# Performance work log

Measured on AMD Instinct MI355X. Metric: run time of the kernel, lower is better.

The kernel has to match this reference:

```python
import jax, jax.numpy as jnp
import numpy as np

N_NODES = 100000
N_EDGES = 3200000
IN_C = 128
OUT_C = 40
NEG_SLOPE = 0.2


def _p(key, shape, scale=0.1):
    return jax.random.normal(key, shape, dtype=jnp.float32) * scale


def setup_inputs() -> dict:
    key = jax.random.key(0)
    ks = jax.random.split(key, 16)
    x = jax.random.normal(ks[0], (N_NODES, IN_C), dtype=jnp.float32)
    edge_index = jax.random.randint(ks[1], (2, N_EDGES), 0, N_NODES, dtype=jnp.int32)
    # layer 1: in=128 -> heads=4, out=4 (concat -> 16)
    W1 = _p(ks[2], (IN_C, 4 * 4))
    a_src1 = _p(ks[3], (4, 4))
    a_dst1 = _p(ks[4], (4, 4))
    b1 = jnp.zeros((16,), jnp.float32)
    # layer 2: 16 -> heads=8, out=8 (concat -> 64)
    W2 = _p(ks[5], (16, 8 * 8))
    a_src2 = _p(ks[6], (8, 8))
    a_dst2 = _p(ks[7], (8, 8))
    b2 = jnp.zeros((64,), jnp.float32)
    # layer 3: 64 -> heads=1, out=OUT_C, concat=False
    W3 = _p(ks[8], (64, OUT_C))
    a_src3 = _p(ks[9], (1, OUT_C))
    a_dst3 = _p(ks[10], (1, OUT_C))
    b3 = jnp.zeros((OUT_C,), jnp.float32)
    return {"x": x, "edge_index": edge_index,
            "W1": W1, "a_src1": a_src1, "a_dst1": a_dst1, "b1": b1,
            "W2": W2, "a_src2": a_src2, "a_dst2": a_dst2, "b2": b2,
            "W3": W3, "a_src3": a_src3, "a_dst3": a_dst3, "b3": b3}


def gat_conv(x, src, dst, W, a_src, a_dst, b, heads, out_c, concat):
    # x: [N, F_in]; src/dst: [E] (self loops already included)
    N = x.shape[0]
    h = (x @ W).reshape(N, heads, out_c)                 # [N, H, C]
    e_src = jnp.sum(h * a_src, axis=-1)                  # [N, H]
    e_dst = jnp.sum(h * a_dst, axis=-1)                  # [N, H]
    e = jax.nn.leaky_relu(e_src[src] + e_dst[dst], NEG_SLOPE)  # [E, H]
    # segment softmax over edges grouped by destination node
    m = jax.ops.segment_max(e, dst, num_segments=N)      # [N, H]
    ex = jnp.exp(e - m[dst])
    s = jax.ops.segment_sum(ex, dst, num_segments=N)
    alpha = ex / (s[dst] + 1e-16)                        # [E, H]
    out = jax.ops.segment_sum(h[src] * alpha[:, :, None], dst, num_segments=N)  # [N, H, C]
    out = out.reshape(N, heads * out_c) if concat else out.mean(axis=1)
    return out + b


def reference(x, edge_index, W1, a_src1, a_dst1, b1, W2, a_src2, a_dst2, b2, W3, a_src3, a_dst3, b3):
    N = x.shape[0]
    loops = jnp.arange(N, dtype=edge_index.dtype)
    src = jnp.concatenate([edge_index[0], loops])
    dst = jnp.concatenate([edge_index[1], loops])
    h = jax.nn.elu(gat_conv(x, src, dst, W1, a_src1, a_dst1, b1, 4, 4, True))
    h = jax.nn.elu(gat_conv(h, src, dst, W2, a_src2, a_dst2, b2, 8, 8, True))
    out = gat_conv(h, src, dst, W3, a_src3, a_dst3, b3, 1, OUT_C, False)
    return out
```

## Files before the change

kernel.cpp:

```cpp
#include <hip/hip_runtime.h>

#define NN 100000
#define NE 3200000
#define ET (NE + NN)
#define NEG_SLOPE 0.2f
#define BSH 7
#define WIN (1 << BSH)
#define NBUC ((NN + WIN - 1) >> BSH)
#define NBLK 256
#define EPB ((ET + NBLK - 1) / NBLK)

__device__ __host__ __forceinline__ int swz(int b) {
    return (b & 7) * (NBLK / 8) + (b >> 3);
}

__device__ __forceinline__ float lrelu(float v) { return v > 0.f ? v : NEG_SLOPE * v; }

__device__ __forceinline__ unsigned short f2bf(float x) {
    unsigned u = __float_as_uint(x);
    return (unsigned short)((u + 0x7fffu + ((u >> 16) & 1u)) >> 16);
}
__device__ __forceinline__ float bflo(unsigned u) { return __uint_as_float(u << 16); }
__device__ __forceinline__ float bfhi(unsigned u) { return __uint_as_float(u & 0xffff0000u); }


template <int FIN, int FOUT, int C>
__device__ __forceinline__ void gemm_attn_body(
    int idx, const float* __restrict__ x, const float* Ws,
    const float* __restrict__ a_src, const float* __restrict__ a_dst,
    unsigned short* __restrict__ h, float* __restrict__ esrc,
    float* __restrict__ edst, int N) {
    constexpr int HH = FOUT / C;
    constexpr int F4 = FOUT / 4;
    constexpr int TPH = C / 4;
    if (idx >= N * F4) return;
    int n = idx / F4, f4 = idx - n * F4;
    int fb = 4 * f4;
    const float4* xr = (const float4*)(x + (long)n * FIN);
    float a0 = 0.f, a1 = 0.f, a2 = 0.f, a3 = 0.f;
#pragma unroll
    for (int k4 = 0; k4 < FIN / 4; ++k4) {
        float4 xv = xr[k4];
        const float* wr = &Ws[(4 * k4) * FOUT + fb];
        float4 w0 = *(const float4*)(wr);
        float4 w1 = *(const float4*)(wr + FOUT);
        float4 w2 = *(const float4*)(wr + 2 * FOUT);
        float4 w3 = *(const float4*)(wr + 3 * FOUT);
        a0 = fmaf(xv.x, w0.x, a0); a1 = fmaf(xv.x, w0.y, a1);
        a2 = fmaf(xv.x, w0.z, a2); a3 = fmaf(xv.x, w0.w, a3);
        a0 = fmaf(xv.y, w1.x, a0); a1 = fmaf(xv.y, w1.y, a1);
        a2 = fmaf(xv.y, w1.z, a2); a3 = fmaf(xv.y, w1.w, a3);
        a0 = fmaf(xv.z, w2.x, a0); a1 = fmaf(xv.z, w2.y, a1);
        a2 = fmaf(xv.z, w2.z, a2); a3 = fmaf(xv.z, w2.w, a3);
        a0 = fmaf(xv.w, w3.x, a0); a1 = fmaf(xv.w, w3.y, a1);
        a2 = fmaf(xv.w, w3.z, a2); a3 = fmaf(xv.w, w3.w, a3);
    }
    unsigned short b0 = f2bf(a0), b1 = f2bf(a1), b2 = f2bf(a2), b3 = f2bf(a3);
    *(ushort4*)(h + (long)n * FOUT + fb) = make_ushort4(b0, b1, b2, b3);
    float q0 = bflo((unsigned)b0), q1 = bflo((unsigned)b1);
    float q2 = bflo((unsigned)b2), q3 = bflo((unsigned)b3);
    float vs = q0 * a_src[fb] + q1 * a_src[fb + 1] + q2 * a_src[fb + 2] + q3 * a_src[fb + 3];
    float vd = q0 * a_dst[fb] + q1 * a_dst[fb + 1] + q2 * a_dst[fb + 2] + q3 * a_dst[fb + 3];
#pragma unroll
    for (int o = 1; o < TPH; o <<= 1) {
        vs += __shfl_xor(vs, o);
        vd += __shfl_xor(vd, o);
    }
    if ((f4 % TPH) == 0) {
        int hh = f4 / TPH;
        esrc[n * HH + hh] = vs;
        edst[n * HH + hh] = vd;
    }
}


__global__ __launch_bounds__(256) void cntgemm_kernel(
    const int* __restrict__ dst, int* __restrict__ cnt,
    const float* __restrict__ x, const float* __restrict__ W,
    const float* __restrict__ a_src, const float* __restrict__ a_dst,
    unsigned short* __restrict__ h, float* __restrict__ esrc,
    float* __restrict__ edst, int N) {
    __shared__ __align__(16) char smem[128 * 16 * 4];
    if (blockIdx.x < NBLK) {
        int* hh = (int*)smem;
        for (int i = threadIdx.x; i < NBUC; i += 256) hh[i] = 0;
        __syncthreads();
        int lo = blockIdx.x * EPB;
        int hi = lo + EPB; if (hi > ET) hi = ET;
        for (int k = lo + threadIdx.x; k < hi; k += 256) {
            int d = (k < NE) ? dst[k] : k - NE;
            atomicAdd(&hh[d >> BSH], 1);
        }
        __syncthreads();
        int col = swz(blockIdx.x);
        for (int i = threadIdx.x; i < NBUC; i += 256)
            cnt[i * NBLK + col] = hh[i];
    } else {
        float* Ws = (float*)smem;
        for (int i = threadIdx.x; i < 128 * 16; i += 256) Ws[i] = W[i];
        __syncthreads();
        int idx = (blockIdx.x - NBLK) * 256 + threadIdx.x;
        gemm_attn_body<128, 16, 4>(idx, x, Ws, a_src, a_dst, h, esrc, edst, N);
    }
}


__global__ __launch_bounds__(256) void rowsum_kernel(const int* __restrict__ cnt,
                                                     int* __restrict__ tot) {
    int wave = threadIdx.x >> 6, lane = threadIdx.x & 63;
    int b = blockIdx.x * 4 + wave;
    if (b >= NBUC) return;
    int4 v = ((const int4*)(cnt + b * NBLK))[lane];
    int s = v.x + v.y + v.z + v.w;
#pragma unroll
    for (int off = 32; off; off >>= 1) s += __shfl_xor(s, off);
    if (lane == 0) tot[b] = s;
}

__global__ __launch_bounds__(1024) void scan_kernel(const int* __restrict__ tot,
                                                    int* __restrict__ bstart) {
    __shared__ int t[1024];
    int b = threadIdx.x;
    int s = (b < NBUC) ? tot[b] : 0;
    t[b] = s;
    __syncthreads();
    for (int off = 1; off < 1024; off <<= 1) {
        int v = (b >= off) ? t[b - off] : 0;
        __syncthreads();
        t[b] += v;
        __syncthreads();
    }
    if (b < NBUC) bstart[b] = t[b] - s;
    if (b == 0) bstart[NBUC] = ET;
}

__global__ __launch_bounds__(256) void base_kernel(int* __restrict__ cnt,
                                                   const int* __restrict__ bstart) {
    int wave = threadIdx.x >> 6, lane = threadIdx.x & 63;
    int b = blockIdx.x * 4 + wave;
    if (b >= NBUC) return;
    int run = bstart[b];
    for (int c0 = 0; c0 < NBLK; c0 += 64) {
        int v = cnt[b * NBLK + c0 + lane];
        int x = v;
#pragma unroll
        for (int off = 1; off < 64; off <<= 1) {
            int y = __shfl_up(x, off);
            if (lane >= off) x += y;
        }
        cnt[b * NBLK + c0 + lane] = run + x - v;
        run += __shfl(x, 63);
    }
}

__global__ __launch_bounds__(1024) void scatter_kernel(const int* __restrict__ src,
                                                       const int* __restrict__ dst,
                                                       const int* __restrict__ base,
                                                       unsigned* __restrict__ tmpp) {
    __shared__ int loff[NBUC];
    int col = swz(blockIdx.x);
    for (int i = threadIdx.x; i < NBUC; i += 1024) loff[i] = base[i * NBLK + col];
    __syncthreads();
    int lo = blockIdx.x * EPB;
    int hi = lo + EPB; if (hi > ET) hi = ET;
    for (int k = lo + threadIdx.x; k < hi; k += 1024) {
        int s, d;
        if (k < NE) { s = src[k]; d = dst[k]; }
        else { s = d = k - NE; }
        int p = atomicAdd(&loff[d >> BSH], 1);
        tmpp[p] = (unsigned)s | ((unsigned)(d & (WIN - 1)) << 17);
    }
}

__global__ __launch_bounds__(1024) void sort_kernel(const int* __restrict__ bstart,
                                                    const unsigned* __restrict__ tmpp,
                                                    int* __restrict__ rowptr,
                                                    int* __restrict__ ssrc) {
    __shared__ int hist[WIN];
    __shared__ int scan[WIN];
    __shared__ int cur[WIN];
    int buc = blockIdx.x;
    int nlo = buc << BSH;
    int nwin = NN - nlo; if (nwin > WIN) nwin = WIN;
    int lo = bstart[buc], hi = bstart[buc + 1];
    int tid = threadIdx.x;
    if (tid < WIN) hist[tid] = 0;
    __syncthreads();
    for (int k = lo + tid; k < hi; k += 1024)
        atomicAdd(&hist[tmpp[k] >> 17], 1);
    __syncthreads();
    if (tid < WIN) scan[tid] = hist[tid];
    __syncthreads();
    for (int off = 1; off < WIN; off <<= 1) {
        int v = (tid >= off && tid < WIN) ? scan[tid - off] : 0;
        __syncthreads();
        if (tid < WIN) scan[tid] += v;
        __syncthreads();
    }
    if (tid < WIN) {
        int ex = scan[tid] - hist[tid];
        cur[tid] = ex;
        if (tid < nwin) rowptr[nlo + tid] = lo + ex;
    }
    if (buc == 0 && tid == 0) rowptr[NN] = ET;
    __syncthreads();
    for (int k = lo + tid; k < hi; k += 1024) {
        unsigned e = tmpp[k];
        int p = atomicAdd(&cur[e >> 17], 1);
        ssrc[lo + p] = (int)(e & 0x1FFFFu);
    }
}


template <int FIN, int FOUT, int C>
__global__ __launch_bounds__(256) void gemm_attn_kernel(
    const float* __restrict__ x, const float* __restrict__ W,
    const float* __restrict__ a_src, const float* __restrict__ a_dst,
    unsigned short* __restrict__ h, float* __restrict__ esrc,
    float* __restrict__ edst, int N) {
    __shared__ __align__(16) float Ws[FIN * FOUT];
    for (int i = threadIdx.x; i < FIN * FOUT; i += blockDim.x) Ws[i] = W[i];
    __syncthreads();
    int idx = blockIdx.x * blockDim.x + threadIdx.x;
    gemm_attn_body<FIN, FOUT, C>(idx, x, Ws, a_src, a_dst, h, esrc, edst, N);
}

template <int FIN, int FOUT, int SO>
__global__ __launch_bounds__(256) void gemm_kernel(const float* __restrict__ x,
                                                   const float* __restrict__ W,
                                                   unsigned short* __restrict__ h, int N) {
    constexpr int F4 = FOUT / 4;
    __shared__ __align__(16) float Ws[FIN * FOUT];
    for (int i = threadIdx.x; i < FIN * FOUT; i += blockDim.x) Ws[i] = W[i];
    __syncthreads();
    int idx = blockIdx.x * blockDim.x + threadIdx.x;
    if (idx >= N * F4) return;
    int n = idx / F4, f4 = idx - n * F4;
    int fb = 4 * f4;
    const float4* xr = (const float4*)(x + (long)n * FIN);
    float a0 = 0.f, a1 = 0.f, a2 = 0.f, a3 = 0.f;
#pragma unroll
    for (int k4 = 0; k4 < FIN / 4; ++k4) {
        float4 xv = xr[k4];
        const float* wr = &Ws[(4 * k4) * FOUT + fb];
        float4 w0 = *(const float4*)(wr);
        float4 w1 = *(const float4*)(wr + FOUT);
        float4 w2 = *(const float4*)(wr + 2 * FOUT);
        float4 w3 = *(const float4*)(wr + 3 * FOUT);
        a0 = fmaf(xv.x, w0.x, a0); a1 = fmaf(xv.x, w0.y, a1);
        a2 = fmaf(xv.x, w0.z, a2); a3 = fmaf(xv.x, w0.w, a3);
        a0 = fmaf(xv.y, w1.x, a0); a1 = fmaf(xv.y, w1.y, a1);
        a2 = fmaf(xv.y, w1.z, a2); a3 = fmaf(xv.y, w1.w, a3);
        a0 = fmaf(xv.z, w2.x, a0); a1 = fmaf(xv.z, w2.y, a1);
        a2 = fmaf(xv.z, w2.z, a2); a3 = fmaf(xv.z, w2.w, a3);
        a0 = fmaf(xv.w, w3.x, a0); a1 = fmaf(xv.w, w3.y, a1);
        a2 = fmaf(xv.w, w3.z, a2); a3 = fmaf(xv.w, w3.w, a3);
    }
    *(ushort4*)(h + (long)n * SO + fb) = make_ushort4(f2bf(a0), f2bf(a1), f2bf(a2), f2bf(a3));
}

template <int C, int SO>
__global__ void attn_kernel(const unsigned short* __restrict__ h,
                            const float* __restrict__ a_src,
                            const float* __restrict__ a_dst, float* __restrict__ esrc,
                            float* __restrict__ edst, int N) {
    int idx = blockIdx.x * blockDim.x + threadIdx.x;
    if (idx >= N) return;
    const uint4* hp = (const uint4*)(h + (long)idx * SO);
    float s = 0.f, d = 0.f;
#pragma unroll
    for (int c8 = 0; c8 < C / 8; ++c8) {
        uint4 v = hp[c8];
        int c = 8 * c8;
        s += bflo(v.x) * a_src[c] + bfhi(v.x) * a_src[c + 1];
        d += bflo(v.x) * a_dst[c] + bfhi(v.x) * a_dst[c + 1];
        s += bflo(v.y) * a_src[c + 2] + bfhi(v.y) * a_src[c + 3];
        d += bflo(v.y) * a_dst[c + 2] + bfhi(v.y) * a_dst[c + 3];
        s += bflo(v.z) * a_src[c + 4] + bfhi(v.z) * a_src[c + 5];
        d += bflo(v.z) * a_dst[c + 4] + bfhi(v.z) * a_dst[c + 5];
        s += bflo(v.w) * a_src[c + 6] + bfhi(v.w) * a_src[c + 7];
        d += bflo(v.w) * a_dst[c + 6] + bfhi(v.w) * a_dst[c + 7];
    }
    esrc[idx] = s;
    edst[idx] = d;
}

template <int H, int C, int L, int G, int NPW, int FPL, int RSL, int U, bool ELU>
__global__ __launch_bounds__(256) void agg_kernel(
    const int* __restrict__ rowptr, const int* __restrict__ ssrc,
    const float* __restrict__ esrc, const float* __restrict__ edst,
    const unsigned short* __restrict__ hbuf, const float* __restrict__ b,
    float* __restrict__ out, int N) {
    constexpr int F = H * C;
    constexpr int AQ = (F + FPL - 1) / FPL;
    constexpr int S = L * G;
    static_assert(S * NPW == 64, "wave layout");
    static_assert(AQ <= L, "lanes cover features");
    int lane = threadIdx.x & 63;
    int wave = threadIdx.x >> 6;
    int sub = lane / S;
    int ls = lane - sub * S;
    int g = ls / L, q = ls - g * L;
    int n = (blockIdx.x * 4 + wave) * NPW + sub;
    if (n >= N) return;
    const bool act = (q < AQ);
    int h = act ? (FPL * q) / C : 0;
    int qa = act ? q : 0;
    float edn = edst[n * H + h];
    int beg = rowptr[n], end = rowptr[n + 1];
    int kend = end - 1;
    float sum = 0.f;
    float acc[FPL];
#pragma unroll
    for (int i = 0; i < FPL; ++i) acc[i] = 0.f;

    int k = beg + g;
    int ss[U];
#pragma unroll
    for (int u = 0; u < U; ++u) {
        int kk = k + u * G;
        ss[u] = ssrc[kk < kend ? kk : kend];
    }
    while (k < end) {
        uint4 hv4[U];
        uint2 hv2[U];
        float es[U];
#pragma unroll
        for (int u = 0; u < U; ++u) {
            if constexpr (FPL == 8) hv4[u] = ((const uint4*)hbuf)[ss[u] * RSL + qa];
            else hv2[u] = ((const uint2*)hbuf)[ss[u] * RSL + qa];
            es[u] = esrc[ss[u] * H + h];
        }
        int kn = k + U * G;
        int sn[U];
#pragma unroll
        for (int u = 0; u < U; ++u) {
            int kk = kn + u * G;
            sn[u] = ssrc[kk < kend ? kk : kend];
        }
        __builtin_amdgcn_sched_barrier(0);
#pragma unroll
        for (int u = 0; u < U; ++u) {
            float ex = (act && (k + u * G < end)) ? __expf(lrelu(es[u] + edn)) : 0.f;
            if constexpr (FPL == 8) {
                uint4 v = hv4[u];
                acc[0] = fmaf(ex, bflo(v.x), acc[0]); acc[1] = fmaf(ex, bfhi(v.x), acc[1]);
                acc[2] = fmaf(ex, bflo(v.y), acc[2]); acc[3] = fmaf(ex, bfhi(v.y), acc[3]);
                acc[4] = fmaf(ex, bflo(v.z), acc[4]); acc[5] = fmaf(ex, bfhi(v.z), acc[5]);
                acc[6] = fmaf(ex, bflo(v.w), acc[6]); acc[7] = fmaf(ex, bfhi(v.w), acc[7]);
            } else {
                uint2 v = hv2[u];
                acc[0] = fmaf(ex, bflo(v.x), acc[0]); acc[1] = fmaf(ex, bfhi(v.x), acc[1]);
                acc[2] = fmaf(ex, bflo(v.y), acc[2]); acc[3] = fmaf(ex, bfhi(v.y), acc[3]);
            }
            sum += ex;
        }
#pragma unroll
        for (int u = 0; u < U; ++u) ss[u] = sn[u];
        k = kn;
    }
#pragma unroll
    for (int step = L; step < S; step <<= 1) {
        sum += __shfl_xor(sum, step);
#pragma unroll
        for (int i = 0; i < FPL; ++i) acc[i] += __shfl_xor(acc[i], step);
    }
    if (g == 0 && act) {
        float inv = 1.f / (sum + 1e-16f);
        float v[FPL];
#pragma unroll
        for (int i = 0; i < FPL; ++i) {
            v[i] = acc[i] * inv + b[FPL * q + i];
            if (ELU) v[i] = v[i] > 0.f ? v[i] : __expf(v[i]) - 1.f;
        }
        float* op = out + n * F + FPL * q;
#pragma unroll
        for (int i = 0; i < FPL; i += 4)
            *(float4*)(op + i) = make_float4(v[i], v[i + 1], v[i + 2], v[i + 3]);
    }
}

static inline int cdiv(long a, int b) { return (int)((a + b - 1) / b); }

extern "C" void kernel_launch(void* const* d_in, const int* in_sizes, int n_in,
                              void* d_out, int out_size, void* d_ws, size_t ws_size,
                              hipStream_t stream) {
    const float* x1 = (const float*)d_in[0];
    const int* ei = (const int*)d_in[1];
    const int* src = ei;
    const int* dst = ei + NE;
    const float* W1 = (const float*)d_in[2];
    const float* as1 = (const float*)d_in[3];
    const float* ad1 = (const float*)d_in[4];
    const float* b1 = (const float*)d_in[5];
    const float* W2 = (const float*)d_in[6];
    const float* as2 = (const float*)d_in[7];
    const float* ad2 = (const float*)d_in[8];
    const float* b2 = (const float*)d_in[9];
    const float* W3 = (const float*)d_in[10];
    const float* as3 = (const float*)d_in[11];
    const float* ad3 = (const float*)d_in[12];
    const float* b3 = (const float*)d_in[13];
    float* out = (float*)d_out;

    char* wsb = (char*)d_ws;
    unsigned short* hbuf = (unsigned short*)wsb;  wsb += (long)NN * 64 * 2;
    float* x2 = (float*)wsb;         wsb += (long)NN * 16 * 4;
    float* x3 = (float*)wsb;         wsb += (long)NN * 64 * 4;
    float* esrc = (float*)wsb;       wsb += (long)NN * 8 * 4;
    float* edst = (float*)wsb;       wsb += (long)NN * 8 * 4;
    unsigned* tmpp = (unsigned*)wsb; wsb += (long)ET * 4;
    int* ssrc = (int*)wsb;           wsb += (long)ET * 4;
    int* rowptr = (int*)wsb;         wsb += (long)(NN + 1) * 4;
    int* cnt = (int*)wsb;            wsb += (long)NBUC * NBLK * 4;
    int* bstart = (int*)wsb;         wsb += (long)(NBUC + 1) * 4;
    int* tot = (int*)wsb;            wsb += (long)NBUC * 4;

    const int B = 256;

    cntgemm_kernel<<<NBLK + cdiv((long)NN * 4, B), B, 0, stream>>>(
        dst, cnt, x1, W1, as1, ad1, hbuf, esrc, edst, NN);
    rowsum_kernel<<<cdiv(NBUC, 4), B, 0, stream>>>(cnt, tot);
    scan_kernel<<<1, 1024, 0, stream>>>(tot, bstart);
    base_kernel<<<cdiv(NBUC, 4), B, 0, stream>>>(cnt, bstart);
    scatter_kernel<<<NBLK, 1024, 0, stream>>>(src, dst, cnt, tmpp);
    sort_kernel<<<NBUC, 1024, 0, stream>>>(bstart, tmpp, rowptr, ssrc);

    agg_kernel<4, 4, 4, 8, 2, 4, 4, 6, true><<<cdiv(NN, 8), B, 0, stream>>>(
        rowptr, ssrc, esrc, edst, hbuf, b1, x2, NN);

    gemm_attn_kernel<16, 64, 8><<<cdiv((long)NN * 16, B), B, 0, stream>>>(
        x2, W2, as2, ad2, hbuf, esrc, edst, NN);
    agg_kernel<8, 8, 8, 8, 1, 8, 8, 6, true><<<cdiv(NN, 4), B, 0, stream>>>(
        rowptr, ssrc, esrc, edst, hbuf, b2, x3, NN);

    gemm_kernel<64, 40, 40><<<cdiv((long)NN * 10, B), B, 0, stream>>>(x3, W3, hbuf, NN);
    attn_kernel<40, 40><<<cdiv(NN, B), B, 0, stream>>>(hbuf, as3, ad3, esrc, edst, NN);
    agg_kernel<1, 40, 8, 8, 1, 8, 5, 6, false><<<cdiv(NN, 4), B, 0, stream>>>(
        rowptr, ssrc, esrc, edst, hbuf, b3, out, NN);
}
```

Measured before the change: 430.3 us.

## Use packed FMA in aggregation, per-wave sort histograms, smaller unroll

The aggregation kernels now accumulate into two-wide float vectors through an elementwise FMA builtin, so the compiler can emit packed FP32 FMA instructions. The sort kernel gives each wave its own histogram copy to reduce LDS atomic contention, then sums the copies before the scan. The aggregation unroll depth drops from 6 to 5, which lowers register pressure but leaves fewer gathers in flight.

Measured after the change: 420.1 us. -2.4%, faster.

```diff
diff --git a/kernel.cpp b/kernel.cpp
--- a/kernel.cpp
+++ b/kernel.cpp
@@ -22,6 +22,18 @@
 }
 __device__ __forceinline__ float bflo(unsigned u) { return __uint_as_float(u << 16); }
 __device__ __forceinline__ float bfhi(unsigned u) { return __uint_as_float(u & 0xffff0000u); }
+
+typedef float f32x2 __attribute__((ext_vector_type(2)));
+__device__ __forceinline__ f32x2 pkfma(f32x2 a, f32x2 b, f32x2 c) {
+#if __has_builtin(__builtin_elementwise_fma)
+    return __builtin_elementwise_fma(a, b, c);
+#else
+    f32x2 r; r.x = fmaf(a.x, b.x, c.x); r.y = fmaf(a.y, b.y, c.y); return r;
+#endif
+}
+__device__ __forceinline__ f32x2 bfpair(unsigned u) {
+    f32x2 r; r.x = bflo(u); r.y = bfhi(u); return r;
+}
 
 
 template <int FIN, int FOUT, int C>
@@ -176,7 +188,7 @@
                                                     const unsigned* __restrict__ tmpp,
                                                     int* __restrict__ rowptr,
                                                     int* __restrict__ ssrc) {
-    __shared__ int hist[WIN];
+    __shared__ int histw[16][WIN];
     __shared__ int scan[WIN];
     __shared__ int cur[WIN];
     int buc = blockIdx.x;
@@ -184,12 +196,20 @@
     int nwin = NN - nlo; if (nwin > WIN) nwin = WIN;
     int lo = bstart[buc], hi = bstart[buc + 1];
     int tid = threadIdx.x;
-    if (tid < WIN) hist[tid] = 0;
+    int wv = tid >> 6;
+    for (int i = tid; i < 16 * WIN; i += 1024) ((int*)histw)[i] = 0;
     __syncthreads();
     for (int k = lo + tid; k < hi; k += 1024)
-        atomicAdd(&hist[tmpp[k] >> 17], 1);
-    __syncthreads();
-    if (tid < WIN) scan[tid] = hist[tid];
+        atomicAdd(&histw[wv][tmpp[k] >> 17], 1);
+    __syncthreads();
+    int myh = 0;
+    if (tid < WIN) {
+        int s = 0;
+#pragma unroll
+        for (int w = 0; w < 16; ++w) s += histw[w][tid];
+        myh = s;
+        scan[tid] = s;
+    }
     __syncthreads();
     for (int off = 1; off < WIN; off <<= 1) {
         int v = (tid >= off && tid < WIN) ? scan[tid - off] : 0;
@@ -198,7 +218,7 @@
         __syncthreads();
     }
     if (tid < WIN) {
-        int ex = scan[tid] - hist[tid];
+        int ex = scan[tid] - myh;
         cur[tid] = ex;
         if (tid < nwin) rowptr[nlo + tid] = lo + ex;
     }
@@ -294,6 +314,7 @@
     constexpr int F = H * C;
     constexpr int AQ = (F + FPL - 1) / FPL;
     constexpr int S = L * G;
+    constexpr int P = FPL / 2;
     static_assert(S * NPW == 64, "wave layout");
     static_assert(AQ <= L, "lanes cover features");
     int lane = threadIdx.x & 63;
@@ -310,9 +331,9 @@
     int beg = rowptr[n], end = rowptr[n + 1];
     int kend = end - 1;
     float sum = 0.f;
-    float acc[FPL];
-#pragma unroll
-    for (int i = 0; i < FPL; ++i) acc[i] = 0.f;
+    f32x2 acc[P];
+#pragma unroll
+    for (int i = 0; i < P; ++i) { acc[i].x = 0.f; acc[i].y = 0.f; }
 
     int k = beg + g;
     int ss[U];
@@ -342,16 +363,17 @@
 #pragma unroll
         for (int u = 0; u < U; ++u) {
             float ex = (act && (k + u * G < end)) ? __expf(lrelu(es[u] + edn)) : 0.f;
+            f32x2 exv; exv.x = ex; exv.y = ex;
             if constexpr (FPL == 8) {
                 uint4 v = hv4[u];
-                acc[0] = fmaf(ex, bflo(v.x), acc[0]); acc[1] = fmaf(ex, bfhi(v.x), acc[1]);
-                acc[2] = fmaf(ex, bflo(v.y), acc[2]); acc[3] = fmaf(ex, bfhi(v.y), acc[3]);
-                acc[4] = fmaf(ex, bflo(v.z), acc[4]); acc[5] = fmaf(ex, bfhi(v.z), acc[5]);
-                acc[6] = fmaf(ex, bflo(v.w), acc[6]); acc[7] = fmaf(ex, bfhi(v.w), acc[7]);
+                acc[0] = pkfma(exv, bfpair(v.x), acc[0]);
+                acc[1] = pkfma(exv, bfpair(v.y), acc[1]);
+                acc[2] = pkfma(exv, bfpair(v.z), acc[2]);
+                acc[3] = pkfma(exv, bfpair(v.w), acc[3]);
             } else {
                 uint2 v = hv2[u];
-                acc[0] = fmaf(ex, bflo(v.x), acc[0]); acc[1] = fmaf(ex, bfhi(v.x), acc[1]);
-                acc[2] = fmaf(ex, bflo(v.y), acc[2]); acc[3] = fmaf(ex, bfhi(v.y), acc[3]);
+                acc[0] = pkfma(exv, bfpair(v.x), acc[0]);
+                acc[1] = pkfma(exv, bfpair(v.y), acc[1]);
             }
             sum += ex;
         }
@@ -363,14 +385,18 @@
     for (int step = L; step < S; step <<= 1) {
         sum += __shfl_xor(sum, step);
 #pragma unroll
-        for (int i = 0; i < FPL; ++i) acc[i] += __shfl_xor(acc[i], step);
+        for (int i = 0; i < P; ++i) {
+            acc[i].x += __shfl_xor(acc[i].x, step);
+            acc[i].y += __shfl_xor(acc[i].y, step);
+        }
     }
     if (g == 0 && act) {
         float inv = 1.f / (sum + 1e-16f);
         float v[FPL];
 #pragma unroll
         for (int i = 0; i < FPL; ++i) {
-            v[i] = acc[i] * inv + b[FPL * q + i];
+            float av = (i & 1) ? acc[i >> 1].y : acc[i >> 1].x;
+            v[i] = av * inv + b[FPL * q + i];
             if (ELU) v[i] = v[i] > 0.f ? v[i] : __expf(v[i]) - 1.f;
         }
         float* op = out + n * F + FPL * q;
@@ -426,16 +452,16 @@
     scatter_kernel<<<NBLK, 1024, 0, stream>>>(src, dst, cnt, tmpp);
     sort_kernel<<<NBUC, 1024, 0, stream>>>(bstart, tmpp, rowptr, ssrc);
 
-    agg_kernel<4, 4, 4, 8, 2, 4, 4, 6, true><<<cdiv(NN, 8), B, 0, stream>>>(
+    agg_kernel<4, 4, 4, 8, 2, 4, 4, 5, true><<<cdiv(NN, 8), B, 0, stream>>>(
         rowptr, ssrc, esrc, edst, hbuf, b1, x2, NN);
 
     gemm_attn_kernel<16, 64, 8><<<cdiv((long)NN * 16, B), B, 0, stream>>>(
         x2, W2, as2, ad2, hbuf, esrc, edst, NN);
-    agg_kernel<8, 8, 8, 8, 1, 8, 8, 6, true><<<cdiv(NN, 4), B, 0, stream>>>(
+    agg_kernel<8, 8, 8, 8, 1, 8, 8, 5, true><<<cdiv(NN, 4), B, 0, stream>>>(
         rowptr, ssrc, esrc, edst, hbuf, b2, x3, NN);
 
     gemm_kernel<64, 40, 40><<<cdiv((long)NN * 10, B), B, 0, stream>>>(x3, W3, hbuf, NN);
     attn_kernel<40, 40><<<cdiv(NN, B), B, 0, stream>>>(hbuf, as3, ad3, esrc, edst, NN);
-    agg_kernel<1, 40, 8, 8, 1, 8, 5, 6, false><<<cdiv(NN, 4), B, 0, stream>>>(
+    agg_kernel<1, 40, 8, 8, 1, 8, 5, 5, false><<<cdiv(NN, 4), B, 0, stream>>>(
         rowptr, ssrc, esrc, edst, hbuf, b3, out, NN);
 }
```
